# Kernel optimization log

Measured on AMD Instinct MI355X. Metric: run time of the kernel, lower is better.

The kernel has to match this reference:

```python
import jax, jax.numpy as jnp
import numpy as np

NUM_SAMPLE = 10   # self._num, hard-coded as range(10) in prob_sample
FSCALE = 5        # neighbor-count kernel
CSCALE = 3        # constraint-count kernel
EPS = 1e-16


def _sum_window(x, k):
    # x: [N,H,W] -> SAME-padded k x k box sum == F.conv2d with ones(1,1,k,k), padding=(k-1)//2
    return jax.lax.reduce_window(x, 0.0, jax.lax.add, (1, k, k), (1, 1, 1), 'SAME')


def _dilate8(x):
    # 3x3 max-pool = one step of 8-connectivity dilation (skimage flood_fill default
    # connectivity for 2D is full connectivity when my_connectivity is None)
    return jax.lax.reduce_window(x, 0.0, jax.lax.max, (1, 3, 3), (1, 1, 1), 'SAME')


def _flood_fill(fg, seed_r, seed_c):
    # fg: [N,H,W] binary float; returns the fg-connected component containing the seed,
    # via fixed-point iteration of masked dilation (equivalent to skimage.flood_fill
    # seeded at the max-neighbor pixel, then thresholding the filled value).
    N, H, W = fg.shape
    reach0 = jnp.zeros_like(fg).at[jnp.arange(N), seed_r, seed_c].set(1.0) * fg

    def cond(st):
        _, changed, it = st
        return changed & (it < H * W)

    def body(st):
        reach, _, it = st
        new = jnp.maximum(reach, _dilate8(reach) * fg)
        return new, jnp.any(new > reach), it + 1

    reach, _, _ = jax.lax.while_loop(cond, body, (reach0, jnp.array(True), jnp.int32(0)))
    return reach


def connectivity_rewards(sample_ns, fg_num):
    # sample_ns: [n, S, H, W] int class indices. Returns binary rewards [n, S, H, W]
    # (reward_type='binary', run_state='train'). All (image, sample) pairs processed
    # in one batched flood fill per foreground class.
    n, S, H, W = sample_ns.shape
    flat = sample_ns.reshape(n * S, H, W)
    total = jnp.zeros((n * S, H, W), jnp.float32)
    for class_idx in range(1, fg_num):  # small fixed loop over fg classes
        fg = (flat == class_idx).astype(jnp.float32)
        neigh = _sum_window(fg, FSCALE) * fg           # count_neighbor * fg
        neigh_flat = neigh.reshape(n * S, H * W)
        seed = jnp.argmax(neigh_flat, axis=-1)          # pixel with max neighbor count
        has_fg = (jnp.max(neigh_flat, axis=-1) > 0).astype(jnp.float32)
        fill = _flood_fill(fg, seed // W, seed % W) * has_fg[:, None, None]
        Fc = _sum_window(fill, CSCALE) * fill           # F_fg_neigbors
        Sc = _sum_window(fg, CSCALE) * fg               # S_fg_neigbors
        r = (jnp.where(Fc == 0, -1.0, Fc) == jnp.where(Sc == 0, -2.0, Sc)).astype(jnp.float32)
        total = total + r
    return total.reshape(n, S, H, W)


def setup_inputs() -> dict:
    key = jax.random.key(0)
    logits = jax.random.normal(key, (4, 4, 512, 512), dtype=jnp.float32)
    preds = jax.nn.softmax(logits, axis=1)  # per-pixel class probabilities [n,c,h,w]
    return {"preds": preds}


def reference(preds):
    n, c, h, w = preds.shape
    skey = jax.random.key(42)
    # prob_sample: per-pixel multinomial over classes, repeated NUM_SAMPLE times
    lg = jnp.moveaxis(jnp.log(preds + EPS), 1, -1)  # [n,h,w,c]
    samp = jax.random.categorical(skey, lg, axis=-1, shape=(NUM_SAMPLE, n, h, w))
    sample_ns = jnp.transpose(samp, (1, 0, 2, 3)).astype(jnp.int32)  # [n,S,h,w]
    prob_ns = jnp.take_along_axis(preds, sample_ns, axis=1)          # [n,S,h,w]
    rewards = jax.lax.stop_gradient(connectivity_rewards(sample_ns, c))
    # REINFORCE objective: maximize reward-weighted log-prob of sampled labelings
    loss = -(rewards * jnp.log(prob_ns + EPS)).mean()
    return loss
```

## Files before the change

### kernel.cpp

```cpp
#include <hip/hip_runtime.h>
#include <stdint.h>

#define JAX_PARTITIONABLE 1

#define SNUM 10
#define NBATCH 4
#define NCLS 4
#define HH 512
#define WW 512
#define IMG (HH*WW)
#define NPIX (SNUM*NBATCH*IMG)
#define GUMTOT ((uint32_t)NPIX*NCLS)
#define HALFG (GUMTOT/2u)
#define WPI (IMG/32)
#define QCAP 3584

#if __has_builtin(__builtin_amdgcn_alignbit)
__device__ __forceinline__ uint32_t rotl32(uint32_t x, int r) {
  return __builtin_amdgcn_alignbit(x, x, (uint32_t)(32 - r));
}
#else
__device__ __forceinline__ uint32_t rotl32(uint32_t x, int r) {
  return (x << r) | (x >> (32 - r));
}
#endif

__device__ __forceinline__ void tf2x32(uint32_t x0, uint32_t x1,
                                       uint32_t& o0, uint32_t& o1) {
  const uint32_t k0 = 0u, k1 = 42u;
  const uint32_t k2 = k0 ^ k1 ^ 0x1BD11BDAu;
  x0 += k0; x1 += k1;
#define TFR(r) { x0 += x1; x1 = rotl32(x1, (r)); x1 ^= x0; }
  TFR(13) TFR(15) TFR(26) TFR(6)
  x0 += k1; x1 += k2 + 1u;
  TFR(17) TFR(29) TFR(16) TFR(24)
  x0 += k2; x1 += k0 + 2u;
  TFR(13) TFR(15) TFR(26) TFR(6)
  x0 += k0; x1 += k1 + 3u;
  TFR(17) TFR(29) TFR(16) TFR(24)
  x0 += k1; x1 += k2 + 4u;
  TFR(13) TFR(15) TFR(26) TFR(6)
  x0 += k2; x1 += k0 + 5u;
#undef TFR
  o0 = x0; o1 = x1;
}

__device__ __forceinline__ float u01(uint32_t bits) {
  const float f = __uint_as_float((bits >> 9) | 0x3f800000u) - 1.0f;
  return fmaxf(f, 1.17549435e-38f);
}

__device__ __forceinline__ uint32_t gum_bits(uint32_t g) {
#if JAX_PARTITIONABLE
  uint32_t y0, y1;
  tf2x32(0u, g, y0, y1);
  return y0 ^ y1;
#else
  uint32_t y0, y1;
  uint32_t j = (g < HALFG) ? g : (g - HALFG);
  tf2x32(j, j + HALFG, y0, y1);
  return (g < HALFG) ? y0 : y1;
#endif
}

__device__ __forceinline__ uint32_t unpack32(uint64_t v) {
  uint64_t tt = v | (v >> 1);
  uint64_t u = ~tt & 0x5555555555555555ULL;
  u = (u ^ (u >> 1))  & 0x3333333333333333ULL;
  u = (u ^ (u >> 2))  & 0x0F0F0F0F0F0F0F0FULL;
  u = (u ^ (u >> 4))  & 0x00FF00FF00FF00FFULL;
  u = (u ^ (u >> 8))  & 0x0000FFFF0000FFFFULL;
  u = (u ^ (u >> 16)) & 0x00000000FFFFFFFFULL;
  return (uint32_t)u;
}

__global__ __launch_bounds__(256) void k_sample(const float* __restrict__ preds,
                                                uint8_t* __restrict__ packed,
                                                float* __restrict__ acc,
                                                uint32_t* __restrict__ gkey,
                                                uint32_t* __restrict__ misc) {
  const int t = blockIdx.x * 256 + threadIdx.x;
  if (t == 0) acc[0] = 0.0f;
  if (t < 120) gkey[t] = 0u;
  if (t == 120) misc[0] = 0u;
  const int sn = t >> 16;
  const int n  = sn & 3;
  const int pg = t & 65535;
  const int pix = pg << 2;

  float pp[NCLS][4];
#pragma unroll
  for (int c = 0; c < NCLS; ++c) {
    const float4 v = *reinterpret_cast<const float4*>(
        preds + (((int64_t)(n * NCLS + c)) << 18) + pix);
    pp[c][0] = v.x; pp[c][1] = v.y; pp[c][2] = v.z; pp[c][3] = v.w;
  }

  const uint32_t gb = (uint32_t)sn * 1048576u + ((uint32_t)pix << 2);
  uint32_t byte = 0;
#pragma unroll
  for (int j = 0; j < 4; ++j) {
    float bp = pp[0][j];
    float bl = __log2f(u01(gum_bits(gb + (uint32_t)(j * 4))));
    int bc = 0;
#pragma unroll
    for (int c = 1; c < NCLS; ++c) {
      const float lc = __log2f(u01(gum_bits(gb + (uint32_t)(j * 4 + c))));
      if (pp[c][j] * bl < bp * lc) { bp = pp[c][j]; bl = lc; bc = c; }
    }
    byte |= (uint32_t)bc << (2 * j);
  }
  packed[t] = (uint8_t)byte;
}

__global__ __launch_bounds__(256) void k_argmax(const uint8_t* __restrict__ packed,
                                                uint32_t* __restrict__ gkey) {
  __shared__ uint32_t sfg[36 * 16];
  __shared__ uint32_t skey;
  const int tid = threadIdx.x;
  const int b = blockIdx.x;
  const int prob = b >> 4;
  const int slab = b & 15;
  const int sn = prob % 40;
  const int k  = 1 + prob / 40;
  if (tid == 0) skey = 0u;

  const uint64_t* p64 = reinterpret_cast<const uint64_t*>(packed);
  const uint64_t pat = (uint64_t)k * 0x5555555555555555ULL;
  const int gr0 = slab * 32 - 2;
  for (int wi = tid; wi < 36 * 16; wi += 256) {
    const int gr = gr0 + (wi >> 4);
    uint32_t m = 0;
    if (gr >= 0 && gr < HH)
      m = unpack32(p64[(int64_t)sn * WPI + (gr << 4) + (wi & 15)] ^ pat);
    sfg[wi] = m;
  }
  __syncthreads();

  uint32_t lbest = 0;
  for (int idx = tid; idx < 512; idx += 256) {
    const int rl = 2 + (idx >> 4);
    const int col = idx & 15;
    const uint32_t cw = sfg[(rl << 4) + col];
    if (!cw) continue;
    uint64_t rb[5];
#pragma unroll
    for (int d = 0; d < 5; ++d) {
      const int base = ((rl + d - 2) << 4) + col;
      const uint32_t le = (col > 0)  ? sfg[base - 1] : 0u;
      const uint32_t cu = sfg[base];
      const uint32_t ri = (col < 15) ? sfg[base + 1] : 0u;
      rb[d] = ((uint64_t)(ri & 7u) << 34) | ((uint64_t)cu << 2) | (uint64_t)(le >> 30);
    }
    const int gr = slab * 32 + (idx >> 4);
    uint32_t bits = cw;
    while (bits) {
      const int j = __ffs(bits) - 1;
      bits &= bits - 1;
      int cnt = 0;
#pragma unroll
      for (int d = 0; d < 5; ++d)
        cnt += __popc((uint32_t)(rb[d] >> j) & 0x1fu);
      const uint32_t fidx = (uint32_t)((gr << 9) + (col << 5) + j);
      const uint32_t key = ((uint32_t)cnt << 18) | (0x3FFFFu - fidx);
      lbest = lbest > key ? lbest : key;
    }
  }
#pragma unroll
  for (int off = 32; off > 0; off >>= 1) {
    const uint32_t o = (uint32_t)__shfl_down((int)lbest, off, 64);
    lbest = lbest > o ? lbest : o;
  }
  if ((threadIdx.x & 63) == 0 && lbest) atomicMax(&skey, lbest);
  __syncthreads();
  if (tid == 0 && skey) atomicMax(&gkey[prob], skey);
}


__device__ __forceinline__ uint32_t runmask(uint32_t m, uint32_t s) {
  uint32_t out = 0;
  while (s) {
    const int j = __ffs(s) - 1;
    const uint32_t bj = 1u << j;
    const uint32_t up = ((m + bj) ^ m) & m;
    const uint32_t rm = __brev(m);
    const uint32_t rbj = 1u << (31 - j);
    const uint32_t dn = __brev(((rm + rbj) ^ rm) & rm);
    const uint32_t run = up | dn;
    out |= run;
    s &= ~run;
  }
  return out;
}

__device__ __forceinline__ void claimf(uint32_t* fg, uint32_t* qw, uint32_t* qb,
                                       uint32_t* qtail, uint32_t t, uint32_t want) {
  const uint32_t old = atomicAnd(&fg[t], ~want);
  uint32_t nb = old & want;
  if (!nb) return;
  const uint32_t ext = runmask(old, nb) & ~nb;
  if (ext) {
    const uint32_t old2 = atomicAnd(&fg[t], ~ext);
    nb |= old2 & ext;
  }
  const uint32_t slot = atomicAdd(qtail, 1u);
  if (slot < QCAP) { qw[slot] = t; qb[slot] = nb; }
}

__device__ __forceinline__ uint64_t shup64(uint64_t v) {
  const uint32_t lo = __shfl_up((unsigned int)v, 1, 64);
  const uint32_t hi = __shfl_up((unsigned int)(v >> 32), 1, 64);
  return ((uint64_t)hi << 32) | lo;
}
__device__ __forceinline__ uint64_t shdn64(uint64_t v) {
  const uint32_t lo = __shfl_down((unsigned int)v, 1, 64);
  const uint32_t hi = __shfl_down((unsigned int)(v >> 32), 1, 64);
  return ((uint64_t)hi << 32) | lo;
}

__global__ __launch_bounds__(64) void k_fill(const float* __restrict__ preds,
                                             const uint8_t* __restrict__ packed,
                                             const uint32_t* __restrict__ gkey,
                                             uint32_t* __restrict__ misc,
                                             float* __restrict__ acc,
                                             float* __restrict__ out) {
  __shared__ uint32_t fg[WPI];
  __shared__ uint32_t qw[QCAP];
  __shared__ uint32_t qb[QCAP];
  __shared__ uint32_t qtail;
  const int tid = threadIdx.x;
  const int prob = blockIdx.x;
  const int sn = prob % 40;
  const int k  = 1 + prob / 40;
  const int n  = sn & 3;
  uint32_t* filldone = misc + 0;

  const uint32_t bkey = gkey[prob];
  float local = 0.0f;
  if ((bkey >> 18) != 0u) {
    const uint32_t seed = 0x3FFFFu - (bkey & 0x3FFFFu);
    const int sr = (int)(seed >> 9), sc = (int)(seed & 511);
    const float* chan = preds + (((int64_t)n) * NCLS + k) * (int64_t)IMG;
    const uint64_t* p64 = reinterpret_cast<const uint64_t*>(packed);
    const uint64_t pat = (uint64_t)k * 0x5555555555555555ULL;

    int r0 = sr - 31; if (r0 < 0) r0 = 0; if (r0 > HH - 64) r0 = HH - 64;
    int cl = (sc >> 5) - (((sc & 31) < 16) ? 1 : 0);
    if (cl < 0) cl = 0; if (cl > 14) cl = 14;
    const int ar = r0 + tid;
    const int64_t pb = (int64_t)sn * WPI + (ar << 4) + cl;
    const uint64_t fgw = ((uint64_t)unpack32(p64[pb + 1] ^ pat) << 32)
                       |            unpack32(p64[pb]     ^ pat);
    uint64_t fill = (ar == sr) ? (1ULL << (sc - (cl << 5))) : 0ULL;

    bool conv = false;
    for (int it = 0; it < 2048; ++it) {
      uint64_t up = shup64(fill); if (tid == 0)  up = 0ULL;
      uint64_t dn = shdn64(fill); if (tid == 63) dn = 0ULL;
      const uint64_t sp = fill | up | dn;
      const uint64_t nf = (fgw & (sp | (sp << 1) | (sp >> 1))) | fill;
      const bool ch = (nf != fill);
      fill = nf;
      if (__ballot(ch) == 0ULL) { conv = true; break; }
    }

    bool esc = !conv;
    if (fill) {
      if (tid == 0 && r0 > 0) esc = true;
      if (tid == 63 && r0 + 63 < HH - 1) esc = true;
      if ((fill & 1ULL) && cl > 0) esc = true;
      if ((fill >> 63) && cl < 14) esc = true;
    }

    if (__ballot(esc) == 0ULL) {
      uint64_t bits = fill;
      const float* rowp = chan + (int64_t)ar * WW + (cl << 5);
      while (bits) {
        const int j = __ffsll((unsigned long long)bits) - 1;
        bits &= bits - 1;
        local += logf(rowp[j] + 1e-16f);
      }
    } else {
      if (tid == 0) qtail = 0u;
      for (int wi = tid; wi < WPI; wi += 64)
        fg[wi] = unpack32(p64[(int64_t)sn * WPI + wi] ^ pat);
      __syncthreads();
      claimf(fg, qw, qb, &qtail, seed >> 5, 1u << (seed & 31));
      uint32_t head = 0;
      while (true) {
        uint32_t tail = atomicAdd(&qtail, 0u);
        if (tail > QCAP) tail = QCAP;
        if (head >= tail) break;
        for (uint32_t i = head + (uint32_t)tid; i < tail; i += 64) {
          const uint32_t w = qw[i], got = qb[i];
          const int row = (int)(w >> 4), cb = (int)(w & 15);
          const uint32_t spread = got | (got << 1) | (got >> 1);
          const bool lo = (got & 1u) != 0u, hi = (got >> 31) != 0u;
          if (row > 0) {
            claimf(fg, qw, qb, &qtail, w - 16, spread);
            if (cb > 0 && lo)  claimf(fg, qw, qb, &qtail, w - 17, 0x80000000u);
            if (cb < 15 && hi) claimf(fg, qw, qb, &qtail, w - 15, 1u);
          }
          if (row < HH - 1) {
            claimf(fg, qw, qb, &qtail, w + 16, spread);
            if (cb > 0 && lo)  claimf(fg, qw, qb, &qtail, w + 15, 0x80000000u);
            if (cb < 15 && hi) claimf(fg, qw, qb, &qtail, w + 17, 1u);
          }
          if (cb > 0 && lo)  claimf(fg, qw, qb, &qtail, w - 1, 0x80000000u);
          if (cb < 15 && hi) claimf(fg, qw, qb, &qtail, w + 1, 1u);
        }
        head = tail;
      }
      uint32_t tot = qtail; if (tot > QCAP) tot = QCAP;
      for (uint32_t i = (uint32_t)tid; i < tot; i += 64) {
        const uint32_t w = qw[i];
        uint32_t bits = qb[i];
        const int row = (int)(w >> 4);
        const int colb = (int)(w & 15) << 5;
        const float* rowp = chan + (int64_t)row * WW;
        while (bits) {
          const int j = __ffs(bits) - 1;
          bits &= bits - 1;
          local += logf(rowp[colb + j] + 1e-16f);
        }
      }
    }
  }

#pragma unroll
  for (int off = 32; off > 0; off >>= 1)
    local += __shfl_down(local, off, 64);
  if (tid == 0) {
    if (local != 0.0f) atomicAdd(acc, local);
    __threadfence();
    const uint32_t old = atomicAdd(filldone, 1u);
    if (old == 119u) {
      const float s = atomicAdd(acc, 0.0f);
      out[0] = -s / 10485760.0f;
    }
  }
}

extern "C" void kernel_launch(void* const* d_in, const int* in_sizes, int n_in,
                              void* d_out, int out_size, void* d_ws, size_t ws_size,
                              hipStream_t stream) {
  const float* preds = (const float*)d_in[0];
  float* out = (float*)d_out;
  char* ws = (char*)d_ws;
  float*    acc    = (float*)ws;
  uint32_t* gkey   = (uint32_t*)(ws + 64);
  uint32_t* misc   = (uint32_t*)(ws + 1536);
  uint8_t*  packed = (uint8_t*)(ws + 4096);

  k_sample<<<10240, 256, 0, stream>>>(preds, packed, acc, gkey, misc);
  k_argmax<<<1920, 256, 0, stream>>>(packed, gkey);
  k_fill<<<120, 64, 0, stream>>>(preds, packed, gkey, misc, acc, out);
}
```

Measured before the change: 160.6 us.

## Fuse seed argmax into flood-fill kernel with 1024-thread blocks and shared fg

Merges the per-problem argmax kernel into the fill kernel. Each of the 120 blocks now unpacks the whole foreground bitmap into shared memory with 1024 threads, computes the max-neighbor seed locally, and then runs the existing 64-thread wavefront flood fill and BFS fallback on the shared bitmap. This removes one kernel launch, the global gkey round trip and the redundant re-unpacking in the fallback path. In exchange, argmax work that previously ran on 1920 blocks now runs on only 120 blocks, so parallelism drops for that phase and 15 of 16 waves sit idle during the fill.

```diff
diff --git a/kernel.cpp b/kernel.cpp
--- a/kernel.cpp
+++ b/kernel.cpp
@@ -77,12 +77,9 @@
 __global__ __launch_bounds__(256) void k_sample(const float* __restrict__ preds,
                                                 uint8_t* __restrict__ packed,
                                                 float* __restrict__ acc,
-                                                uint32_t* __restrict__ gkey,
                                                 uint32_t* __restrict__ misc) {
   const int t = blockIdx.x * 256 + threadIdx.x;
-  if (t == 0) acc[0] = 0.0f;
-  if (t < 120) gkey[t] = 0u;
-  if (t == 120) misc[0] = 0u;
+  if (t == 0) { acc[0] = 0.0f; misc[0] = 0u; }
   const int sn = t >> 16;
   const int n  = sn & 3;
   const int pg = t & 65535;
@@ -111,69 +108,6 @@
     byte |= (uint32_t)bc << (2 * j);
   }
   packed[t] = (uint8_t)byte;
-}
-
-__global__ __launch_bounds__(256) void k_argmax(const uint8_t* __restrict__ packed,
-                                                uint32_t* __restrict__ gkey) {
-  __shared__ uint32_t sfg[36 * 16];
-  __shared__ uint32_t skey;
-  const int tid = threadIdx.x;
-  const int b = blockIdx.x;
-  const int prob = b >> 4;
-  const int slab = b & 15;
-  const int sn = prob % 40;
-  const int k  = 1 + prob / 40;
-  if (tid == 0) skey = 0u;
-
-  const uint64_t* p64 = reinterpret_cast<const uint64_t*>(packed);
-  const uint64_t pat = (uint64_t)k * 0x5555555555555555ULL;
-  const int gr0 = slab * 32 - 2;
-  for (int wi = tid; wi < 36 * 16; wi += 256) {
-    const int gr = gr0 + (wi >> 4);
-    uint32_t m = 0;
-    if (gr >= 0 && gr < HH)
-      m = unpack32(p64[(int64_t)sn * WPI + (gr << 4) + (wi & 15)] ^ pat);
-    sfg[wi] = m;
-  }
-  __syncthreads();
-
-  uint32_t lbest = 0;
-  for (int idx = tid; idx < 512; idx += 256) {
-    const int rl = 2 + (idx >> 4);
-    const int col = idx & 15;
-    const uint32_t cw = sfg[(rl << 4) + col];
-    if (!cw) continue;
-    uint64_t rb[5];
-#pragma unroll
-    for (int d = 0; d < 5; ++d) {
-      const int base = ((rl + d - 2) << 4) + col;
-      const uint32_t le = (col > 0)  ? sfg[base - 1] : 0u;
-      const uint32_t cu = sfg[base];
-      const uint32_t ri = (col < 15) ? sfg[base + 1] : 0u;
-      rb[d] = ((uint64_t)(ri & 7u) << 34) | ((uint64_t)cu << 2) | (uint64_t)(le >> 30);
-    }
-    const int gr = slab * 32 + (idx >> 4);
-    uint32_t bits = cw;
-    while (bits) {
-      const int j = __ffs(bits) - 1;
-      bits &= bits - 1;
-      int cnt = 0;
-#pragma unroll
-      for (int d = 0; d < 5; ++d)
-        cnt += __popc((uint32_t)(rb[d] >> j) & 0x1fu);
-      const uint32_t fidx = (uint32_t)((gr << 9) + (col << 5) + j);
-      const uint32_t key = ((uint32_t)cnt << 18) | (0x3FFFFu - fidx);
-      lbest = lbest > key ? lbest : key;
-    }
-  }
-#pragma unroll
-  for (int off = 32; off > 0; off >>= 1) {
-    const uint32_t o = (uint32_t)__shfl_down((int)lbest, off, 64);
-    lbest = lbest > o ? lbest : o;
-  }
-  if ((threadIdx.x & 63) == 0 && lbest) atomicMax(&skey, lbest);
-  __syncthreads();
-  if (tid == 0 && skey) atomicMax(&gkey[prob], skey);
 }
 
 
@@ -218,39 +152,80 @@
   return ((uint64_t)hi << 32) | lo;
 }
 
-__global__ __launch_bounds__(64) void k_fill(const float* __restrict__ preds,
-                                             const uint8_t* __restrict__ packed,
-                                             const uint32_t* __restrict__ gkey,
-                                             uint32_t* __restrict__ misc,
-                                             float* __restrict__ acc,
-                                             float* __restrict__ out) {
+__global__ __launch_bounds__(1024) void k_tail(const float* __restrict__ preds,
+                                               const uint8_t* __restrict__ packed,
+                                               uint32_t* __restrict__ misc,
+                                               float* __restrict__ acc,
+                                               float* __restrict__ out) {
   __shared__ uint32_t fg[WPI];
   __shared__ uint32_t qw[QCAP];
   __shared__ uint32_t qb[QCAP];
+  __shared__ uint32_t skey;
   __shared__ uint32_t qtail;
   const int tid = threadIdx.x;
   const int prob = blockIdx.x;
   const int sn = prob % 40;
   const int k  = 1 + prob / 40;
   const int n  = sn & 3;
-  uint32_t* filldone = misc + 0;
-
-  const uint32_t bkey = gkey[prob];
+
+  if (tid == 0) { skey = 0u; qtail = 0u; }
+
+  const uint64_t* p64 = reinterpret_cast<const uint64_t*>(packed);
+  const uint64_t pat = (uint64_t)k * 0x5555555555555555ULL;
+  for (int wi = tid; wi < WPI; wi += 1024)
+    fg[wi] = unpack32(p64[(int64_t)sn * WPI + wi] ^ pat);
+  __syncthreads();
+
+  uint32_t lbest = 0;
+  for (int wi = tid; wi < WPI; wi += 1024) {
+    const uint32_t cw = fg[wi];
+    if (!cw) continue;
+    const int row = wi >> 4, col = wi & 15;
+    uint64_t rb[5];
+#pragma unroll
+    for (int d = 0; d < 5; ++d) {
+      const int rr = row + d - 2;
+      if (rr < 0 || rr >= HH) { rb[d] = 0; continue; }
+      const int base = (rr << 4) + col;
+      const uint32_t le = (col > 0)  ? fg[base - 1] : 0u;
+      const uint32_t cu = fg[base];
+      const uint32_t ri = (col < 15) ? fg[base + 1] : 0u;
+      rb[d] = ((uint64_t)(ri & 7u) << 34) | ((uint64_t)cu << 2) | (uint64_t)(le >> 30);
+    }
+    uint32_t bits = cw;
+    while (bits) {
+      const int j = __ffs(bits) - 1;
+      bits &= bits - 1;
+      int cnt = 0;
+#pragma unroll
+      for (int d = 0; d < 5; ++d)
+        cnt += __popc((uint32_t)(rb[d] >> j) & 0x1fu);
+      const uint32_t key = ((uint32_t)cnt << 18) | (0x3FFFFu - (uint32_t)(wi * 32 + j));
+      lbest = lbest > key ? lbest : key;
+    }
+  }
+#pragma unroll
+  for (int off = 32; off > 0; off >>= 1) {
+    const uint32_t o = (uint32_t)__shfl_down((int)lbest, off, 64);
+    lbest = lbest > o ? lbest : o;
+  }
+  if ((tid & 63) == 0 && lbest) atomicMax(&skey, lbest);
+  __syncthreads();
+  const uint32_t bkey = skey;
+
+  if (tid >= 64) return;
+
   float local = 0.0f;
   if ((bkey >> 18) != 0u) {
     const uint32_t seed = 0x3FFFFu - (bkey & 0x3FFFFu);
     const int sr = (int)(seed >> 9), sc = (int)(seed & 511);
     const float* chan = preds + (((int64_t)n) * NCLS + k) * (int64_t)IMG;
-    const uint64_t* p64 = reinterpret_cast<const uint64_t*>(packed);
-    const uint64_t pat = (uint64_t)k * 0x5555555555555555ULL;
 
     int r0 = sr - 31; if (r0 < 0) r0 = 0; if (r0 > HH - 64) r0 = HH - 64;
     int cl = (sc >> 5) - (((sc & 31) < 16) ? 1 : 0);
     if (cl < 0) cl = 0; if (cl > 14) cl = 14;
     const int ar = r0 + tid;
-    const int64_t pb = (int64_t)sn * WPI + (ar << 4) + cl;
-    const uint64_t fgw = ((uint64_t)unpack32(p64[pb + 1] ^ pat) << 32)
-                       |            unpack32(p64[pb]     ^ pat);
+    const uint64_t fgw = ((uint64_t)fg[(ar << 4) + cl + 1] << 32) | fg[(ar << 4) + cl];
     uint64_t fill = (ar == sr) ? (1ULL << (sc - (cl << 5))) : 0ULL;
 
     bool conv = false;
@@ -281,10 +256,6 @@
         local += logf(rowp[j] + 1e-16f);
       }
     } else {
-      if (tid == 0) qtail = 0u;
-      for (int wi = tid; wi < WPI; wi += 64)
-        fg[wi] = unpack32(p64[(int64_t)sn * WPI + wi] ^ pat);
-      __syncthreads();
       claimf(fg, qw, qb, &qtail, seed >> 5, 1u << (seed & 31));
       uint32_t head = 0;
       while (true) {
@@ -333,7 +304,7 @@
   if (tid == 0) {
     if (local != 0.0f) atomicAdd(acc, local);
     __threadfence();
-    const uint32_t old = atomicAdd(filldone, 1u);
+    const uint32_t old = atomicAdd(misc, 1u);
     if (old == 119u) {
       const float s = atomicAdd(acc, 0.0f);
       out[0] = -s / 10485760.0f;
@@ -348,11 +319,9 @@
   float* out = (float*)d_out;
   char* ws = (char*)d_ws;
   float*    acc    = (float*)ws;
-  uint32_t* gkey   = (uint32_t*)(ws + 64);
-  uint32_t* misc   = (uint32_t*)(ws + 1536);
+  uint32_t* misc   = (uint32_t*)(ws + 64);
   uint8_t*  packed = (uint8_t*)(ws + 4096);
 
-  k_sample<<<10240, 256, 0, stream>>>(preds, packed, acc, gkey, misc);
-  k_argmax<<<1920, 256, 0, stream>>>(packed, gkey);
-  k_fill<<<120, 64, 0, stream>>>(preds, packed, gkey, misc, acc, out);
-}
+  k_sample<<<10240, 256, 0, stream>>>(preds, packed, acc, misc);
+  k_tail<<<120, 1024, 0, stream>>>(preds, packed, misc, acc, out);
+}
```

Result: slower. 173.3 us (+7.9%).
